# Kernel optimization log

Measured on AMD Instinct MI355X. Metric: run time of the kernel, lower is better.

Reference implementation:

```python
import jax, jax.numpy as jnp
import numpy as np

K = 16  # kNN size (self included)
R = 4   # upsampling ratio


def _knn(pts, k):
    # pts: (B,N,3) -> idx (B,N,k); smallest distance first, so idx[:,:,0] is self
    sq = jnp.sum(pts * pts, axis=-1)
    d = sq[:, :, None] - 2.0 * jnp.einsum('bnd,bmd->bnm', pts, pts) + sq[:, None, :]
    _, idx = jax.lax.top_k(-d, k)
    return idx


def _gather(feats, idx):
    # feats (B,N,C), idx (B,N,k) -> (B,N,k,C)
    return jax.vmap(lambda f, i: f[i])(feats, idx)


def _conv1d(x, w, b):  # pointwise Conv1d: x (B,C,N)
    return jnp.einsum('oc,bcn->bon', w, x) + b[None, :, None]


def _conv2d(x, w, b):  # pointwise Conv2d: x (B,C,N,K)
    return jnp.einsum('oc,bcnk->bonk', w, x) + b[None, :, None, None]


def setup_inputs() -> dict:
    key = jax.random.key(0)
    ks = jax.random.split(key, 16)
    B, N = 2, 8192
    w = lambda k, s: jax.random.normal(k, s, jnp.float32) * 0.1
    return {
        'x': jax.random.normal(ks[0], (B, 3, N), jnp.float32),
        'mlp1_w1': w(ks[1], (32, 3)), 'mlp1_b1': jnp.zeros((32,), jnp.float32),
        'mlp1_w2': w(ks[2], (64, 32)), 'mlp1_b2': jnp.zeros((64,), jnp.float32),
        'mlp2_w1': w(ks[3], (32, 9)), 'mlp2_b1': jnp.zeros((32,), jnp.float32),
        'mlp3_w1': w(ks[4], (128, 96)), 'mlp3_b1': jnp.zeros((128,), jnp.float32),
        'mlp3_w2': w(ks[5], (12, 128)), 'mlp3_b2': jnp.zeros((12,), jnp.float32),
        'att_w1': w(ks[6], (128, 64)), 'att_b1': jnp.zeros((128,), jnp.float32),
        'att_w2': w(ks[7], (64, 128)), 'att_b2': jnp.zeros((64,), jnp.float32),
    }


def reference(x, mlp1_w1, mlp1_b1, mlp1_w2, mlp1_b2, mlp2_w1, mlp2_b1,
              mlp3_w1, mlp3_b1, mlp3_w2, mlp3_b2,
              att_w1, att_b1, att_w2, att_b2):
    B, C, N = x.shape
    pts = jnp.transpose(x, (0, 2, 1))                     # (B,N,3)
    idx = _knn(jax.lax.stop_gradient(pts), K)             # (B,N,K)

    # local 3x3 covariance features -> (B,9,N)
    nb = _gather(pts, idx)                                # (B,N,K,3)
    c = nb - jnp.mean(nb, axis=2, keepdims=True)
    cov = jnp.einsum('bnki,bnkj->bnij', c, c) / K         # (B,N,3,3)
    cov_feat = jnp.transpose(cov.reshape(B, N, 9), (0, 2, 1))

    # mlp1: 3 -> 32 -> 64, relu on both (last_act=True)
    f1 = jax.nn.relu(_conv1d(jax.nn.relu(_conv1d(x, mlp1_w1, mlp1_b1)), mlp1_w2, mlp1_b2))

    # gather neighbor features (exclude self) and form relative features
    fk = _gather(jnp.transpose(f1, (0, 2, 1)), idx[:, :, 1:])   # (B,N,K-1,64)
    f_knn = jnp.transpose(fk, (0, 3, 1, 2)) - f1[:, :, :, None]  # (B,64,N,K-1)

    # attention MLP (2D): 64 -> 128 -> 64, softmax over neighbor axis
    h = jax.nn.relu(_conv2d(f_knn, att_w1, att_b1))
    w = jax.nn.softmax(_conv2d(h, att_w2, att_b2), axis=-1)
    f_agg = jnp.sum(w * f_knn, axis=-1)                   # (B,64,N)

    # mlp2: 9 -> 32 with relu
    f_cov = jax.nn.relu(_conv1d(cov_feat, mlp2_w1, mlp2_b1))     # (B,32,N)

    f = jnp.concatenate([f_agg, f_cov], axis=1)           # (B,96,N)
    g = _conv1d(jax.nn.relu(_conv1d(f, mlp3_w1, mlp3_b1)), mlp3_w2, mlp3_b2)  # (B,3R,N)

    return jnp.tile(x, (1, 1, R)) + 0.15 * g.reshape(B, -1, R * N)
```

## Files before the change

### kernel.cpp

```cpp
#include <hip/hip_runtime.h>

#define BB 2
#define NN 8192
#define KK 16
#define QPB 64
#define PRE 256
#define STASH 32
typedef unsigned long long ull;
typedef unsigned short ushort;
#define KINF 0xFFFFFFFFFFFFFFFFULL

typedef __attribute__((ext_vector_type(8))) short short8;
typedef __attribute__((ext_vector_type(4))) float f32x4;

static __device__ __forceinline__ ushort f2bf(float f) {
    unsigned u = __float_as_uint(f);
    unsigned r = (u + 0x7FFFu + ((u >> 16) & 1u)) >> 16;
    return (ushort)r;
}
static __device__ __forceinline__ float bf2f(ushort s) {
    return __uint_as_float(((unsigned)s) << 16);
}

static __device__ __forceinline__ float distq(const float4& qp, const float4& cn) {
    return fmaf(qp.x, cn.x, fmaf(qp.y, cn.y, fmaf(qp.z, cn.z, __fadd_rn(qp.w, cn.w))));
}

__global__ __launch_bounds__(256) void prep_f1_kernel(
    const float* __restrict__ x, float4* __restrict__ pts4, float4* __restrict__ pts4n,
    const float* __restrict__ w1, const float* __restrict__ b1,
    const float* __restrict__ w2, const float* __restrict__ b2,
    ushort* __restrict__ f1)
{
    if (blockIdx.x < 64) {
        int t = blockIdx.x * 256 + threadIdx.x;
        int b = t >> 13, n = t & (NN - 1);
        float x0 = x[(b * 3 + 0) * NN + n];
        float x1 = x[(b * 3 + 1) * NN + n];
        float x2 = x[(b * 3 + 2) * NN + n];
        float sq = fmaf(x2, x2, fmaf(x1, x1, __fmul_rn(x0, x0)));
        pts4[t]  = make_float4(x0, x1, x2, sq);
        pts4n[t] = make_float4(-2.f * x0, -2.f * x1, -2.f * x2, sq);
    } else {
        int P = (blockIdx.x - 64) * 256 + threadIdx.x;
        int b = P >> 13, n = P & (NN - 1);
        float x0 = x[(b * 3 + 0) * NN + n];
        float x1 = x[(b * 3 + 1) * NN + n];
        float x2 = x[(b * 3 + 2) * NN + n];
        float h[32];
#pragma unroll
        for (int o = 0; o < 32; ++o) {
            float v = fmaf(w1[o * 3 + 2], x2, fmaf(w1[o * 3 + 1], x1, fmaf(w1[o * 3 + 0], x0, b1[o])));
            h[o] = fmaxf(v, 0.f);
        }
#pragma unroll
        for (int o4 = 0; o4 < 16; ++o4) {
            float vv[4];
#pragma unroll
            for (int u = 0; u < 4; ++u) {
                int o = o4 * 4 + u;
                float v = b2[o];
#pragma unroll
                for (int k = 0; k < 32; ++k) v = fmaf(w2[o * 32 + k], h[k], v);
                vv[u] = fmaxf(v, 0.f);
            }
            ushort4 s = { f2bf(vv[0]), f2bf(vv[1]), f2bf(vv[2]), f2bf(vv[3]) };
            *(ushort4*)(f1 + (size_t)P * 64 + o4 * 4) = s;
        }
    }
}

__global__ __launch_bounds__(512) void knn_prefix_kernel(
    const float4* __restrict__ pts4, const float4* __restrict__ pts4n,
    float* __restrict__ thrb)
{
    __shared__ float pbuf[11 * 512];
    __shared__ float smem[8 * 4 * 64];

    const int t    = threadIdx.x;
    const int wv   = t >> 6;
    const int lane = t & 63;
    const int b    = blockIdx.y;
    const int q    = blockIdx.x * QPB + lane;
    const int sl   = __builtin_amdgcn_readfirstlane(wv);

    const float4 qp = pts4[b * NN + q];
    const float4* __restrict__ cp = pts4n + (size_t)b * NN + (size_t)sl * 1024;

    float l0 = 3.0e38f, l1 = 3.0e38f, l2 = 3.0e38f, l3 = 3.0e38f;
    float curmax = 3.0e38f;
    int pend = 0;

    for (int i0 = 0; i0 < PRE; i0 += 8) {
#pragma unroll
        for (int u = 0; u < 8; ++u) {
            float d = distq(qp, cp[i0 + u]);
            pbuf[pend * 512 + t] = d;
            pend += (d < curmax) ? 1 : 0;
        }
        if (__any(pend >= 4)) {
            for (int j = 0; j < 11; ++j) {
                if (!__any(j < pend)) break;
                float v = pbuf[j * 512 + t];
                float k = (j < pend) ? v : 3.0e38f;
                bool b3 = k < l3, b2 = k < l2, b1 = k < l1, b0 = k < l0;
                l3 = b3 ? (b2 ? l2 : k) : l3;
                l2 = b2 ? (b1 ? l1 : k) : l2;
                l1 = b1 ? (b0 ? l0 : k) : l1;
                l0 = b0 ? k : l0;
            }
            pend = 0;
            curmax = l3;
        }
    }
    for (int j = 0; j < 11; ++j) {
        if (!__any(j < pend)) break;
        float v = pbuf[j * 512 + t];
        float k = (j < pend) ? v : 3.0e38f;
        bool b3 = k < l3, b2 = k < l2, b1 = k < l1, b0 = k < l0;
        l3 = b3 ? (b2 ? l2 : k) : l3;
        l2 = b2 ? (b1 ? l1 : k) : l2;
        l1 = b1 ? (b0 ? l0 : k) : l1;
        l0 = b0 ? k : l0;
    }

    __syncthreads();
    smem[(wv * 4 + 0) * 64 + lane] = l0;
    smem[(wv * 4 + 1) * 64 + lane] = l1;
    smem[(wv * 4 + 2) * 64 + lane] = l2;
    smem[(wv * 4 + 3) * 64 + lane] = l3;
    __syncthreads();

    if (t < QPB) {
        float h[8];
        int kc[8];
#pragma unroll
        for (int s = 0; s < 8; ++s) { h[s] = smem[(s * 4) * 64 + t]; kc[s] = 0; }
        float best = 3.0e38f;
        for (int o = 0; o < KK; ++o) {
            best = h[0]; int bs = 0;
#pragma unroll
            for (int s = 1; s < 8; ++s) { if (h[s] < best) { best = h[s]; bs = s; } }
#pragma unroll
            for (int s = 0; s < 8; ++s) {
                if (s == bs) {
                    kc[s]++;
                    h[s] = (kc[s] < 4) ? smem[(s * 4 + kc[s]) * 64 + t] : 3.0e38f;
                }
            }
        }
        thrb[(size_t)b * NN + blockIdx.x * QPB + t] = best;
    }
}

__global__ __launch_bounds__(512) void knn_scan_kernel(
    const float4* __restrict__ pts4, const float4* __restrict__ pts4n,
    const float* __restrict__ thrb, unsigned* __restrict__ bufm)
{
    const int t    = threadIdx.x;
    const int wv   = t >> 6;
    const int lane = t & 63;
    const int b    = blockIdx.y;
    const int q    = blockIdx.x * QPB + lane;
    const int s    = __builtin_amdgcn_readfirstlane(blockIdx.z * 8 + wv);

    const float4 qp = pts4[b * NN + q];
    const float thr = thrb[(size_t)b * NN + q];
    const float4* __restrict__ cp = pts4n + (size_t)b * NN + (size_t)s * 256;

    unsigned m[8];
    float4 ca[8], cb[8];
#pragma unroll
    for (int u = 0; u < 8; ++u) ca[u] = cp[u];

#pragma unroll
    for (int wg = 0; wg < 8; ++wg) {
        unsigned w = 0;
#pragma unroll
        for (int u = 0; u < 8; ++u) cb[u] = cp[wg * 32 + 8 + u];
#pragma unroll
        for (int u = 0; u < 8; ++u) {
            float d = distq(qp, ca[u]);
            w |= (d <= thr) ? (1u << u) : 0u;
        }
#pragma unroll
        for (int u = 0; u < 8; ++u) ca[u] = cp[wg * 32 + 16 + u];
#pragma unroll
        for (int u = 0; u < 8; ++u) {
            float d = distq(qp, cb[u]);
            w |= (d <= thr) ? (1u << (8 + u)) : 0u;
        }
#pragma unroll
        for (int u = 0; u < 8; ++u) cb[u] = cp[wg * 32 + 24 + u];
#pragma unroll
        for (int u = 0; u < 8; ++u) {
            float d = distq(qp, ca[u]);
            w |= (d <= thr) ? (1u << (16 + u)) : 0u;
        }
        if (wg < 7) {
#pragma unroll
            for (int u = 0; u < 8; ++u) ca[u] = cp[wg * 32 + 32 + u];
        }
#pragma unroll
        for (int u = 0; u < 8; ++u) {
            float d = distq(qp, cb[u]);
            w |= (d <= thr) ? (1u << (24 + u)) : 0u;
        }
        m[wg] = w;
    }

    const size_t row = (((size_t)b * 32 + s) << 13) + (size_t)blockIdx.x * QPB + lane;
    uint4 lo = make_uint4(m[0], m[1], m[2], m[3]);
    uint4 hi = make_uint4(m[4], m[5], m[6], m[7]);
    *(uint4*)(bufm + row * 8)     = lo;
    *(uint4*)(bufm + row * 8 + 4) = hi;
}

__global__ __launch_bounds__(256) void knn_select_kernel(
    const float4* __restrict__ pts4, const float4* __restrict__ pts4n,
    const unsigned* __restrict__ bufm,
    int* __restrict__ iout)
{
    __shared__ ull sm3[4][8][8][KK];
    __shared__ ushort stash[STASH][256];

    const int t = threadIdx.x;
    const int wv = t >> 6, lane = t & 63;
    const int qq = lane & 7, hh = lane >> 3;
    const int q  = (blockIdx.x * 4 + wv) * 8 + qq;
    const int b  = q >> 13;
    const int ql = q & (NN - 1);

    const float4 qp = pts4[q];
    ull list[KK];
#pragma unroll
    for (int i = 0; i < KK; ++i) list[i] = KINF;

    int pend = 0;
#pragma unroll
    for (int ss = 0; ss < 4; ++ss) {
        const int s = hh * 4 + ss;
        const int cell = ((b * 32 + s) << 13) + ql;
        const ull* __restrict__ mp = (const ull*)(bufm + (size_t)cell * 8);
        const int sb = s * 256;
#pragma unroll
        for (int wd = 0; wd < 4; ++wd) {
            ull w = mp[wd];
            while (w) {
                int bit = __builtin_ctzll(w);
                w &= w - 1;
                int id = sb + wd * 64 + bit;
                if (pend < STASH) {
                    stash[pend][t] = (ushort)id;
                    ++pend;
                } else {
                    float d = distq(qp, pts4n[b * NN + id]);
                    unsigned ud = __float_as_uint(d);
                    ud ^= ((unsigned)((int)ud >> 31)) | 0x80000000u;
                    ull k = ((ull)ud << 32) | (unsigned)id;
#pragma unroll
                    for (int i2 = KK - 1; i2 > 0; --i2) {
                        bool c1 = k < list[i2];
                        bool c2 = k < list[i2 - 1];
                        ull nd = c2 ? list[i2 - 1] : k;
                        list[i2] = c1 ? nd : list[i2];
                    }
                    list[0] = (k < list[0]) ? k : list[0];
                }
            }
        }
    }

    for (int j = 0; ; j += 2) {
        if (!__any(j < pend)) break;
        int j1 = j + 1;
        int id0 = stash[(j  < pend) ? j  : 0][t];
        int id1 = stash[(j1 < pend) ? j1 : 0][t];
        float4 cn0 = pts4n[b * NN + id0];
        float4 cn1 = pts4n[b * NN + id1];

        float d0 = distq(qp, cn0);
        unsigned ud0 = __float_as_uint(d0);
        ud0 ^= ((unsigned)((int)ud0 >> 31)) | 0x80000000u;
        ull k0 = (j < pend) ? ((((ull)ud0) << 32) | (unsigned)id0) : KINF;
#pragma unroll
        for (int i2 = KK - 1; i2 > 0; --i2) {
            bool c1 = k0 < list[i2];
            bool c2 = k0 < list[i2 - 1];
            ull nd = c2 ? list[i2 - 1] : k0;
            list[i2] = c1 ? nd : list[i2];
        }
        list[0] = (k0 < list[0]) ? k0 : list[0];

        float d1 = distq(qp, cn1);
        unsigned ud1 = __float_as_uint(d1);
        ud1 ^= ((unsigned)((int)ud1 >> 31)) | 0x80000000u;
        ull k1 = (j1 < pend) ? ((((ull)ud1) << 32) | (unsigned)id1) : KINF;
#pragma unroll
        for (int i2 = KK - 1; i2 > 0; --i2) {
            bool c1 = k1 < list[i2];
            bool c2 = k1 < list[i2 - 1];
            ull nd = c2 ? list[i2 - 1] : k1;
            list[i2] = c1 ? nd : list[i2];
        }
        list[0] = (k1 < list[0]) ? k1 : list[0];
    }

#pragma unroll
    for (int k = 0; k < KK; ++k) sm3[wv][hh][qq][k] = list[k];

    if (hh == 0) {
        ull h[8]; int kc[8];
#pragma unroll
        for (int s = 0; s < 8; ++s) { h[s] = sm3[wv][s][qq][0]; kc[s] = 0; }
        int* op = iout + (size_t)q * KK;
        for (int o = 0; o < KK; ++o) {
            ull best = h[0]; int bs = 0;
#pragma unroll
            for (int s = 1; s < 8; ++s) { if (h[s] < best) { best = h[s]; bs = s; } }
            op[o] = (int)(unsigned)(best & 0xFFFFFFFFULL);
#pragma unroll
            for (int s = 0; s < 8; ++s) {
                if (s == bs) {
                    kc[s]++;
                    h[s] = (kc[s] < KK) ? sm3[wv][s][qq][kc[s]] : KINF;
                }
            }
        }
    }
}

__global__ __launch_bounds__(256, 2) void attn_cov_kernel(
    const ushort* __restrict__ f1, const int* __restrict__ idx,
    const float* __restrict__ aw1, const float* __restrict__ ab1,
    const float* __restrict__ aw2, const float* __restrict__ ab2,
    ushort* __restrict__ fagg,
    const float4* __restrict__ pts4,
    const float* __restrict__ cw, const float* __restrict__ cb,
    ushort* __restrict__ fcov)
{
    __shared__ __align__(16) ushort w1l[128][72];
    __shared__ __align__(16) ushort w2l[64][136];
    __shared__ __align__(16) ushort fkb[4][16][72];
    __shared__ __align__(16) ushort hb[4][16][136];

    const int t = threadIdx.x;

    if (blockIdx.x >= 512) {
        int P = (blockIdx.x - 512) * 256 + t;
        int b = P >> 13;
        const int4* ip4 = (const int4*)(idx + (size_t)P * KK);
        int ids[KK];
#pragma unroll
        for (int g = 0; g < 4; ++g) {
            int4 v = ip4[g];
            ids[g * 4 + 0] = v.x; ids[g * 4 + 1] = v.y;
            ids[g * 4 + 2] = v.z; ids[g * 4 + 3] = v.w;
        }
        float px[KK], py[KK], pz[KK];
#pragma unroll
        for (int k = 0; k < KK; ++k) {
            float4 c = pts4[b * NN + ids[k]];
            px[k] = c.x; py[k] = c.y; pz[k] = c.z;
        }
        float mx = 0.f, my = 0.f, mz = 0.f;
#pragma unroll
        for (int k = 0; k < KK; ++k) { mx += px[k]; my += py[k]; mz += pz[k]; }
        mx *= (1.f / 16.f); my *= (1.f / 16.f); mz *= (1.f / 16.f);
        float c00 = 0, c01 = 0, c02 = 0, c11 = 0, c12 = 0, c22 = 0;
#pragma unroll
        for (int k = 0; k < KK; ++k) {
            float dx = px[k] - mx, dy = py[k] - my, dz = pz[k] - mz;
            c00 = fmaf(dx, dx, c00); c01 = fmaf(dx, dy, c01); c02 = fmaf(dx, dz, c02);
            c11 = fmaf(dy, dy, c11); c12 = fmaf(dy, dz, c12); c22 = fmaf(dz, dz, c22);
        }
        const float inv = 1.f / 16.f;
        float cf[9] = { c00 * inv, c01 * inv, c02 * inv,
                        c01 * inv, c11 * inv, c12 * inv,
                        c02 * inv, c12 * inv, c22 * inv };
        ushort* outp = fcov + (size_t)P * 32;
#pragma unroll
        for (int o = 0; o < 32; ++o) {
            float v = cb[o];
#pragma unroll
            for (int m = 0; m < 9; ++m) v = fmaf(cw[o * 9 + m], cf[m], v);
            outp[o] = f2bf(fmaxf(v, 0.f));
        }
        return;
    }

    const int wv = t >> 6, lane = t & 63;
    const int l15 = lane & 15, qd = lane >> 4;

    for (int i = t; i < 128 * 64; i += 256) {
        int r = i >> 6, c = i & 63;
        w1l[r][c] = f2bf(aw1[i]);
    }
    for (int i = t; i < 64 * 128; i += 256) {
        int r = i >> 7, c = i & 127;
        w2l[r][c] = f2bf(aw2[i]);
    }
    __syncthreads();

    const int W = blockIdx.x * 4 + wv;
    for (int g = 0; g < 8; ++g) {
        const int P = W * 8 + g;
        const int b = P >> 13;

        float fc = bf2f(f1[(size_t)P * 64 + lane]);
        ushort fn[15];
#pragma unroll
        for (int j = 0; j < 15; ++j) {
            int nb = idx[(size_t)P * KK + 1 + j];
            fn[j] = f1[((size_t)b * NN + nb) * 64 + lane];
        }
#pragma unroll
        for (int j = 0; j < 15; ++j) fkb[wv][j][lane] = f2bf(bf2f(fn[j]) - fc);
        fkb[wv][15][lane] = 0;

        short8 a0 = *(const short8*)&fkb[wv][l15][qd * 8];
        short8 a1 = *(const short8*)&fkb[wv][l15][32 + qd * 8];

#pragma unroll
        for (int tile = 0; tile < 8; ++tile) {
            float bv = ab1[tile * 16 + l15];
            f32x4 acc = { bv, bv, bv, bv };
            short8 b0 = *(const short8*)&w1l[tile * 16 + l15][qd * 8];
            short8 b1f = *(const short8*)&w1l[tile * 16 + l15][32 + qd * 8];
            acc = __builtin_amdgcn_mfma_f32_16x16x32_bf16(a0, b0, acc, 0, 0, 0);
            acc = __builtin_amdgcn_mfma_f32_16x16x32_bf16(a1, b1f, acc, 0, 0, 0);
#pragma unroll
            for (int reg = 0; reg < 4; ++reg)
                hb[wv][qd * 4 + reg][tile * 16 + l15] = f2bf(fmaxf(acc[reg], 0.f));
        }

        short8 a2[4];
#pragma unroll
        for (int ks = 0; ks < 4; ++ks)
            a2[ks] = *(const short8*)&hb[wv][l15][ks * 32 + qd * 8];

        f32x4 L[4];
#pragma unroll
        for (int tile = 0; tile < 4; ++tile) {
            float bv = ab2[tile * 16 + l15];
            f32x4 acc = { bv, bv, bv, bv };
#pragma unroll
            for (int ks = 0; ks < 4; ++ks) {
                short8 bf = *(const short8*)&w2l[tile * 16 + l15][ks * 32 + qd * 8];
                acc = __builtin_amdgcn_mfma_f32_16x16x32_bf16(a2[ks], bf, acc, 0, 0, 0);
            }
            L[tile] = acc;
        }

        float fa[4];
#pragma unroll
        for (int tile = 0; tile < 4; ++tile) {
            float m1 = -3.0e38f;
#pragma unroll
            for (int reg = 0; reg < 4; ++reg)
                if (qd * 4 + reg < 15) m1 = fmaxf(m1, L[tile][reg]);
            m1 = fmaxf(m1, __shfl_xor(m1, 16));
            m1 = fmaxf(m1, __shfl_xor(m1, 32));
            float e[4], ssum = 0.f;
#pragma unroll
            for (int reg = 0; reg < 4; ++reg) {
                bool valid = (qd * 4 + reg < 15);
                e[reg] = valid ? __expf(L[tile][reg] - m1) : 0.f;
                ssum += e[reg];
            }
            ssum += __shfl_xor(ssum, 16);
            ssum += __shfl_xor(ssum, 32);
            float part = 0.f;
#pragma unroll
            for (int reg = 0; reg < 4; ++reg) {
                float fkv = bf2f(fkb[wv][qd * 4 + reg][tile * 16 + l15]);
                part = fmaf(e[reg], fkv, part);
            }
            part += __shfl_xor(part, 16);
            part += __shfl_xor(part, 32);
            fa[tile] = part / ssum;
        }
        if (qd == 0) {
#pragma unroll
            for (int tile = 0; tile < 4; ++tile)
                fagg[(size_t)P * 64 + tile * 16 + l15] = f2bf(fa[tile]);
        }
    }
}

__global__ __launch_bounds__(256) void mlp3_kernel(
    const ushort* __restrict__ fagg, const ushort* __restrict__ fcov,
    const float* __restrict__ w1, const float* __restrict__ b1,
    const float* __restrict__ w2, const float* __restrict__ b2,
    const float* __restrict__ x, float* __restrict__ out)
{
    __shared__ __align__(16) ushort fb[4][16][104];
    __shared__ __align__(16) ushort hb[4][16][136];

    const int t = threadIdx.x;
    const int wv = t >> 6, lane = t & 63;
    const int l15 = lane & 15, qd = lane >> 4;

    short8 w1f[8][3];
#pragma unroll
    for (int tile = 0; tile < 8; ++tile)
#pragma unroll
        for (int ks = 0; ks < 3; ++ks) {
            const float* p = w1 + ((size_t)(tile * 16 + l15) * 96 + ks * 32 + qd * 8);
            float4 A = *(const float4*)p, B = *(const float4*)(p + 4);
            short8 f;
            f[0] = f2bf(A.x); f[1] = f2bf(A.y); f[2] = f2bf(A.z); f[3] = f2bf(A.w);
            f[4] = f2bf(B.x); f[5] = f2bf(B.y); f[6] = f2bf(B.z); f[7] = f2bf(B.w);
            w1f[tile][ks] = f;
        }
    short8 w2f[4];
#pragma unroll
    for (int ks = 0; ks < 4; ++ks) {
        short8 f = {};
        if (l15 < 12) {
            const float* p = w2 + ((size_t)l15 * 128 + ks * 32 + qd * 8);
            float4 A = *(const float4*)p, B = *(const float4*)(p + 4);
            f[0] = f2bf(A.x); f[1] = f2bf(A.y); f[2] = f2bf(A.z); f[3] = f2bf(A.w);
            f[4] = f2bf(B.x); f[5] = f2bf(B.y); f[6] = f2bf(B.z); f[7] = f2bf(B.w);
        }
        w2f[ks] = f;
    }

    const int T = blockIdx.x * 4 + wv;

    {
        const int pt = lane >> 2, c4 = lane & 3;
        const ushort* fap = fagg + ((size_t)(T * 16 + pt) * 64 + c4 * 16);
        *(short8*)&fb[wv][pt][c4 * 16]     = *(const short8*)(fap);
        *(short8*)&fb[wv][pt][c4 * 16 + 8] = *(const short8*)(fap + 8);
        const ushort* fcp = fcov + ((size_t)(T * 16 + pt) * 32 + c4 * 8);
        *(short8*)&fb[wv][pt][64 + c4 * 8] = *(const short8*)(fcp);
    }

    short8 a[3];
#pragma unroll
    for (int ks = 0; ks < 3; ++ks)
        a[ks] = *(const short8*)&fb[wv][l15][ks * 32 + qd * 8];

#pragma unroll
    for (int tile = 0; tile < 8; ++tile) {
        float bv = b1[tile * 16 + l15];
        f32x4 acc = { bv, bv, bv, bv };
#pragma unroll
        for (int ks = 0; ks < 3; ++ks)
            acc = __builtin_amdgcn_mfma_f32_16x16x32_bf16(a[ks], w1f[tile][ks], acc, 0, 0, 0);
#pragma unroll
        for (int reg = 0; reg < 4; ++reg)
            hb[wv][qd * 4 + reg][tile * 16 + l15] = f2bf(fmaxf(acc[reg], 0.f));
    }

    short8 a2[4];
#pragma unroll
    for (int ks = 0; ks < 4; ++ks)
        a2[ks] = *(const short8*)&hb[wv][l15][ks * 32 + qd * 8];

    float bv2 = (l15 < 12) ? b2[l15] : 0.f;
    f32x4 acc = { bv2, bv2, bv2, bv2 };
#pragma unroll
    for (int ks = 0; ks < 4; ++ks)
        acc = __builtin_amdgcn_mfma_f32_16x16x32_bf16(a2[ks], w2f[ks], acc, 0, 0, 0);

    if (l15 < 12) {
        const int c = l15 >> 2, rr = l15 & 3;
#pragma unroll
        for (int reg = 0; reg < 4; ++reg) {
            int P = T * 16 + qd * 4 + reg;
            int b = P >> 13, n = P & (NN - 1);
            float xv = x[((size_t)b * 3 + c) * NN + n];
            out[(((size_t)b * 3 + c) * 4 + rr) * NN + n] = xv + 0.15f * acc[reg];
        }
    }
}

extern "C" void kernel_launch(void* const* d_in, const int* in_sizes, int n_in,
                              void* d_out, int out_size, void* d_ws, size_t ws_size,
                              hipStream_t stream)
{
    (void)in_sizes; (void)n_in; (void)out_size; (void)ws_size;
    const float* x    = (const float*)d_in[0];
    const float* m1w1 = (const float*)d_in[1];
    const float* m1b1 = (const float*)d_in[2];
    const float* m1w2 = (const float*)d_in[3];
    const float* m1b2 = (const float*)d_in[4];
    const float* m2w1 = (const float*)d_in[5];
    const float* m2b1 = (const float*)d_in[6];
    const float* m3w1 = (const float*)d_in[7];
    const float* m3b1 = (const float*)d_in[8];
    const float* m3w2 = (const float*)d_in[9];
    const float* m3b2 = (const float*)d_in[10];
    const float* aw1  = (const float*)d_in[11];
    const float* ab1  = (const float*)d_in[12];
    const float* aw2  = (const float*)d_in[13];
    const float* ab2  = (const float*)d_in[14];
    float* out = (float*)d_out;

    char* ws = (char*)d_ws;
    float4* pts4  = (float4*)(ws + 0);
    float4* pts4n = (float4*)(ws + 262144);
    float*  thrb  = (float*)(ws + 524288);
    int*    idxb  = (int*)  (ws + 589824);
    unsigned* bufm = (unsigned*)(ws + 2686976);
    ushort* f1b   = (ushort*)(ws + 19464192);
    ushort* fagg  = (ushort*)(ws + 21561344);
    ushort* fcov  = (ushort*)(ws + 23658496);

    prep_f1_kernel<<<128, 256, 0, stream>>>(x, pts4, pts4n, m1w1, m1b1, m1w2, m1b2, f1b);
    knn_prefix_kernel<<<dim3(NN / QPB, BB), 512, 0, stream>>>(pts4, pts4n, thrb);
    knn_scan_kernel<<<dim3(NN / QPB, BB, 4), 512, 0, stream>>>(pts4, pts4n, thrb, bufm);
    knn_select_kernel<<<512, 256, 0, stream>>>(pts4, pts4n, bufm, idxb);
    attn_cov_kernel<<<576, 256, 0, stream>>>(f1b, idxb, aw1, ab1, aw2, ab2, fagg,
                                             pts4, m2w1, m2b1, fcov);
    mlp3_kernel<<<256, 256, 0, stream>>>(fagg, fcov, m3w1, m3b1, m3w2, m3b2, x, out);
}
```

Before: 263.3 us.

## Compute kNN candidate distances with bf16 split-precision MFMA in the scan

Reworks the kNN scan so that query-candidate distances come from 16x16x32 bf16 MFMA instructions. Coordinates and squared norms are split into hi/lo bf16 pairs to recover near-fp32 accuracy, and candidate tiles are staged through LDS. The threshold is loosened by a relative factor and an absolute epsilon so that candidates are not lost to rounding, and the exact fp32 recheck in select keeps the result correct. The bitmask layout and grid shape change, and select's bit-to-index decode is updated to match. The looser threshold may send more candidates to the select stage.

```diff
diff --git a/kernel.cpp b/kernel.cpp
--- a/kernel.cpp
+++ b/kernel.cpp
@@ -6,9 +6,11 @@
 #define QPB 64
 #define PRE 256
 #define STASH 32
+#define EPSF 0.02f
 typedef unsigned long long ull;
 typedef unsigned short ushort;
 #define KINF 0xFFFFFFFFFFFFFFFFULL
+#define BFONE 0x3F80
 
 typedef __attribute__((ext_vector_type(8))) short short8;
 typedef __attribute__((ext_vector_type(4))) float f32x4;
@@ -28,6 +30,7 @@
 
 __global__ __launch_bounds__(256) void prep_f1_kernel(
     const float* __restrict__ x, float4* __restrict__ pts4, float4* __restrict__ pts4n,
+    ushort* __restrict__ ptsC64,
     const float* __restrict__ w1, const float* __restrict__ b1,
     const float* __restrict__ w2, const float* __restrict__ b2,
     ushort* __restrict__ f1)
@@ -41,6 +44,23 @@
         float sq = fmaf(x2, x2, fmaf(x1, x1, __fmul_rn(x0, x0)));
         pts4[t]  = make_float4(x0, x1, x2, sq);
         pts4n[t] = make_float4(-2.f * x0, -2.f * x1, -2.f * x2, sq);
+
+        float m2x = -2.f * x0, m2y = -2.f * x1, m2z = -2.f * x2;
+        ushort hx = f2bf(m2x), hy = f2bf(m2y), hz = f2bf(m2z);
+        ushort lx = f2bf(m2x - bf2f(hx));
+        ushort ly = f2bf(m2y - bf2f(hy));
+        ushort lz = f2bf(m2z - bf2f(hz));
+        ushort sh = f2bf(sq), sl = f2bf(sq - bf2f(sh));
+        short8 r0 = { (short)hx, (short)hy, (short)hz, (short)lx,
+                      (short)ly, (short)lz, (short)hx, (short)hy };
+        short8 r1 = { (short)hz, (short)lx, (short)ly, (short)lz,
+                      (short)sh, (short)sl, (short)BFONE, (short)BFONE };
+        short8 zz = { 0, 0, 0, 0, 0, 0, 0, 0 };
+        ushort* cp = ptsC64 + (size_t)t * 32;
+        *(short8*)(cp)      = r0;
+        *(short8*)(cp + 8)  = r1;
+        *(short8*)(cp + 16) = zz;
+        *(short8*)(cp + 24) = zz;
     } else {
         int P = (blockIdx.x - 64) * 256 + threadIdx.x;
         int b = P >> 13, n = P & (NN - 1);
@@ -153,67 +173,74 @@
     }
 }
 
-__global__ __launch_bounds__(512) void knn_scan_kernel(
-    const float4* __restrict__ pts4, const float4* __restrict__ pts4n,
+__global__ __launch_bounds__(256) void knn_scan_kernel(
+    const float4* __restrict__ pts4, const ushort* __restrict__ ptsC64,
     const float* __restrict__ thrb, unsigned* __restrict__ bufm)
 {
+    __shared__ __align__(16) char lbuf[10240];
+
     const int t    = threadIdx.x;
     const int wv   = t >> 6;
     const int lane = t & 63;
+    const int l15  = lane & 15, l4 = lane >> 4;
     const int b    = blockIdx.y;
-    const int q    = blockIdx.x * QPB + lane;
-    const int s    = __builtin_amdgcn_readfirstlane(blockIdx.z * 8 + wv);
-
-    const float4 qp = pts4[b * NN + q];
-    const float thr = thrb[(size_t)b * NN + q];
-    const float4* __restrict__ cp = pts4n + (size_t)b * NN + (size_t)s * 256;
-
-    unsigned m[8];
-    float4 ca[8], cb[8];
-#pragma unroll
-    for (int u = 0; u < 8; ++u) ca[u] = cp[u];
-
-#pragma unroll
-    for (int wg = 0; wg < 8; ++wg) {
-        unsigned w = 0;
-#pragma unroll
-        for (int u = 0; u < 8; ++u) cb[u] = cp[wg * 32 + 8 + u];
-#pragma unroll
-        for (int u = 0; u < 8; ++u) {
-            float d = distq(qp, ca[u]);
-            w |= (d <= thr) ? (1u << u) : 0u;
-        }
-#pragma unroll
-        for (int u = 0; u < 8; ++u) ca[u] = cp[wg * 32 + 16 + u];
-#pragma unroll
-        for (int u = 0; u < 8; ++u) {
-            float d = distq(qp, cb[u]);
-            w |= (d <= thr) ? (1u << (8 + u)) : 0u;
-        }
-#pragma unroll
-        for (int u = 0; u < 8; ++u) cb[u] = cp[wg * 32 + 24 + u];
-#pragma unroll
-        for (int u = 0; u < 8; ++u) {
-            float d = distq(qp, ca[u]);
-            w |= (d <= thr) ? (1u << (16 + u)) : 0u;
-        }
-        if (wg < 7) {
-#pragma unroll
-            for (int u = 0; u < 8; ++u) ca[u] = cp[wg * 32 + 32 + u];
-        }
-#pragma unroll
-        for (int u = 0; u < 8; ++u) {
-            float d = distq(qp, cb[u]);
-            w |= (d <= thr) ? (1u << (24 + u)) : 0u;
-        }
-        m[wg] = w;
-    }
-
-    const size_t row = (((size_t)b * 32 + s) << 13) + (size_t)blockIdx.x * QPB + lane;
-    uint4 lo = make_uint4(m[0], m[1], m[2], m[3]);
-    uint4 hi = make_uint4(m[4], m[5], m[6], m[7]);
-    *(uint4*)(bufm + row * 8)     = lo;
-    *(uint4*)(bufm + row * 8 + 4) = hi;
+    const int z    = blockIdx.z;
+    const int qt   = blockIdx.x * 4 + wv;
+    const int qbase = qt * 16;
+
+    const float4 p = pts4[(size_t)b * NN + qbase + l15];
+    const ushort qhx = f2bf(p.x), qhy = f2bf(p.y), qhz = f2bf(p.z);
+    const ushort qlx = f2bf(p.x - bf2f(qhx));
+    const ushort qly = f2bf(p.y - bf2f(qhy));
+    const ushort qlz = f2bf(p.z - bf2f(qhz));
+    const ushort qsh = f2bf(p.w), qsl = f2bf(p.w - bf2f(qsh));
+    short8 qf;
+    if (l4 == 0)
+        qf = short8{ (short)qhx, (short)qhy, (short)qhz, (short)qhx,
+                     (short)qhy, (short)qhz, (short)qlx, (short)qly };
+    else if (l4 == 1)
+        qf = short8{ (short)qlz, (short)qlx, (short)qly, (short)qlz,
+                     (short)BFONE, (short)BFONE, (short)qsh, (short)qsl };
+    else
+        qf = short8{ 0, 0, 0, 0, 0, 0, 0, 0 };
+
+    const float thrq = thrb[(size_t)b * NN + qbase + l15] * 1.001f + EPSF;
+
+    const uint4* __restrict__ gsrc =
+        (const uint4*)(ptsC64 + ((size_t)b * NN + (size_t)z * 1024) * 32);
+
+    unsigned* __restrict__ op =
+        bufm + (size_t)(b * NN + qbase + l15) * 256 + z * 32 + l4 * 8;
+
+    uint4 r0 = gsrc[t], r1 = gsrc[t + 256];
+    unsigned w4[4];
+
+#pragma unroll 1
+    for (int g = 0; g < 8; ++g) {
+        __syncthreads();
+        *(uint4*)(lbuf + (t >> 2) * 80 + (t & 3) * 16) = r0;
+        *(uint4*)(lbuf + ((t + 256) >> 2) * 80 + (t & 3) * 16) = r1;
+        if (g < 7) {
+            r0 = gsrc[(g + 1) * 512 + t];
+            r1 = gsrc[(g + 1) * 512 + t + 256];
+        }
+        __syncthreads();
+
+        unsigned acc = 0;
+#pragma unroll
+        for (int i = 0; i < 8; ++i) {
+            short8 cf = *(const short8*)(lbuf + (i * 16 + l15) * 80 + l4 * 16);
+            f32x4 D = { 0.f, 0.f, 0.f, 0.f };
+            D = __builtin_amdgcn_mfma_f32_16x16x32_bf16(cf, qf, D, 0, 0, 0);
+            acc = acc * 2u + (unsigned)(D[0] <= thrq);
+            acc = acc * 2u + (unsigned)(D[1] <= thrq);
+            acc = acc * 2u + (unsigned)(D[2] <= thrq);
+            acc = acc * 2u + (unsigned)(D[3] <= thrq);
+        }
+        w4[g & 3] = acc;
+        if ((g & 3) == 3)
+            *(uint4*)(op + (g >> 2) * 4) = make_uint4(w4[0], w4[1], w4[2], w4[3]);
+    }
 }
 
 __global__ __launch_bounds__(256) void knn_select_kernel(
@@ -229,27 +256,28 @@
     const int qq = lane & 7, hh = lane >> 3;
     const int q  = (blockIdx.x * 4 + wv) * 8 + qq;
     const int b  = q >> 13;
-    const int ql = q & (NN - 1);
 
     const float4 qp = pts4[q];
     ull list[KK];
 #pragma unroll
     for (int i = 0; i < KK; ++i) list[i] = KINF;
 
+    const unsigned* __restrict__ mrow = bufm + (size_t)q * 256 + hh * 32;
     int pend = 0;
-#pragma unroll
-    for (int ss = 0; ss < 4; ++ss) {
-        const int s = hh * 4 + ss;
-        const int cell = ((b * 32 + s) << 13) + ql;
-        const ull* __restrict__ mp = (const ull*)(bufm + (size_t)cell * 8);
-        const int sb = s * 256;
-#pragma unroll
-        for (int wd = 0; wd < 4; ++wd) {
-            ull w = mp[wd];
+#pragma unroll 1
+    for (int g4 = 0; g4 < 8; ++g4) {
+        uint4 v = ((const uint4*)mrow)[g4];
+        unsigned wsv[4] = { v.x, v.y, v.z, v.w };
+#pragma unroll
+        for (int j = 0; j < 4; ++j) {
+            unsigned w = wsv[j];
+            const int W = hh * 32 + g4 * 4 + j;
+            const int cb = ((W >> 5) << 10) + ((W & 7) << 7) + (((W >> 3) & 3) << 2);
             while (w) {
-                int bit = __builtin_ctzll(w);
+                int p = __builtin_ctz(w);
                 w &= w - 1;
-                int id = sb + wd * 64 + bit;
+                int m = 31 - p;
+                int id = cb + ((m >> 2) << 4) + (m & 3);
                 if (pend < STASH) {
                     stash[pend][t] = (ushort)id;
                     ++pend;
@@ -600,18 +628,19 @@
     float* out = (float*)d_out;
 
     char* ws = (char*)d_ws;
-    float4* pts4  = (float4*)(ws + 0);
-    float4* pts4n = (float4*)(ws + 262144);
-    float*  thrb  = (float*)(ws + 524288);
-    int*    idxb  = (int*)  (ws + 589824);
+    float4* pts4   = (float4*)(ws + 0);
+    float4* pts4n  = (float4*)(ws + 262144);
+    float*  thrb   = (float*)(ws + 524288);
+    int*    idxb   = (int*)  (ws + 589824);
+    ushort* ptsC64 = (ushort*)(ws + 1638400);
     unsigned* bufm = (unsigned*)(ws + 2686976);
-    ushort* f1b   = (ushort*)(ws + 19464192);
-    ushort* fagg  = (ushort*)(ws + 21561344);
-    ushort* fcov  = (ushort*)(ws + 23658496);
-
-    prep_f1_kernel<<<128, 256, 0, stream>>>(x, pts4, pts4n, m1w1, m1b1, m1w2, m1b2, f1b);
+    ushort* f1b    = (ushort*)(ws + 19464192);
+    ushort* fagg   = (ushort*)(ws + 21561344);
+    ushort* fcov   = (ushort*)(ws + 23658496);
+
+    prep_f1_kernel<<<128, 256, 0, stream>>>(x, pts4, pts4n, ptsC64, m1w1, m1b1, m1w2, m1b2, f1b);
     knn_prefix_kernel<<<dim3(NN / QPB, BB), 512, 0, stream>>>(pts4, pts4n, thrb);
-    knn_scan_kernel<<<dim3(NN / QPB, BB, 4), 512, 0, stream>>>(pts4, pts4n, thrb, bufm);
+    knn_scan_kernel<<<dim3(128, BB, 8), 256, 0, stream>>>(pts4, ptsC64, thrb, bufm);
     knn_select_kernel<<<512, 256, 0, stream>>>(pts4, pts4n, bufm, idxb);
     attn_cov_kernel<<<576, 256, 0, stream>>>(f1b, idxb, aw1, ab1, aw2, ab2, fagg,
                                              pts4, m2w1, m2b1, fcov);
```

Result: faster. 253.7 us (-3.7%).
